# Performance work log

Hardware: AMD Instinct MI355X
Metric: run time of the kernel (lower is better)

## Reference

```python
import jax, jax.numpy as jnp
import numpy as np

DECAY = 0.8
COMMITMENT = 1.0
EPS = 1e-05


def setup_inputs() -> dict:
    key = jax.random.key(0)
    k1, k2, k3 = jax.random.split(key, 3)
    dim, n_embed = 256, 8192
    input = jax.random.normal(k1, (8, 2048, dim), dtype=jnp.float32)
    embed = jax.random.normal(k2, (dim, n_embed), dtype=jnp.float32)
    cluster_size = jnp.zeros((n_embed,), dtype=jnp.float32)
    embed_avg = jax.random.normal(k3, (dim, n_embed), dtype=jnp.float32)
    return {"input": input, "embed": embed, "cluster_size": cluster_size, "embed_avg": embed_avg}


def reference(input, embed, cluster_size, embed_avg):
    dim, n_embed = embed.shape
    flatten = input.reshape(-1, dim)  # [N, d]
    dist = (jnp.sum(flatten * flatten, axis=1, keepdims=True)
            - 2.0 * flatten @ embed
            + jnp.sum(embed * embed, axis=0, keepdims=True))  # [N, C]
    embed_ind_flat = jnp.argmin(dist, axis=1)  # [N]
    embed_ind = embed_ind_flat.reshape(input.shape[:-1])
    quantize = jnp.take(embed.T, embed_ind_flat, axis=0).reshape(input.shape)

    # training-mode EMA codebook update (onehot.sum(0) and x^T @ onehot as segment ops)
    counts = jax.ops.segment_sum(jnp.ones_like(embed_ind_flat, dtype=input.dtype),
                                 embed_ind_flat, num_segments=n_embed)  # [C]
    embed_sum = jax.ops.segment_sum(flatten, embed_ind_flat, num_segments=n_embed).T  # [d, C]
    new_cluster_size = cluster_size * DECAY + counts * (1.0 - DECAY)
    new_embed_avg = embed_avg * DECAY + embed_sum * (1.0 - DECAY)
    smoothed = (new_cluster_size + EPS) / (jnp.sum(new_cluster_size) + n_embed * EPS)
    smoothed = smoothed * jnp.sum(new_cluster_size)
    new_embed = new_embed_avg / smoothed[None, :]

    commit_loss = jnp.mean((quantize - input) ** 2) * COMMITMENT
    # straight-through (no grad here in fwd-only, values identical)
    quantize_st = input + jax.lax.stop_gradient(quantize - input)
    return quantize_st, embed_ind, commit_loss, new_embed, new_cluster_size, new_embed_avg
```

## Files before the change

kernel.cpp:

```cpp
#include <hip/hip_runtime.h>
#include <hip/hip_bf16.h>
#include <float.h>
#include <stdint.h>

#define N_ROWS 16384
#define DIM 256
#define NE 8192
#define K2 768
#define DECAY 0.8f
#define OMD 0.2f
#define EPS 1e-5f
#define NPAN 8
#define PANELC 1024

#define WS_X2     0
#define WS_EMBEDT 0
#define WS_ESUMT  2097152
#define WS_B2T    6291456
#define WS_ENORM  9437184
#define WS_COUNTS 9445376
#define WS_SMOOTH 9453568
#define WS_PV     9461760
#define WS_PI     9592832
#define WS_INDI   9723904
#define WS_LOSS   9740288
#define WS_TOTAL  9740289

#define OUT_Q    0
#define OUT_IND  4194304
#define OUT_LOSS 4210688
#define OUT_NE   4210689
#define OUT_NCS  6307841
#define OUT_NEA  6316033

typedef __attribute__((ext_vector_type(8))) short bf16x8;
typedef __attribute__((ext_vector_type(4))) float f32x4;

static __device__ __forceinline__ ushort f2bf(float f) {
    uint32_t u = __float_as_uint(f);
    uint32_t r = (u + 0x7fffu + ((u >> 16) & 1u)) >> 16;
    return (ushort)r;
}
static __device__ __forceinline__ float bf2f(ushort h) {
    return __uint_as_float(((uint32_t)h) << 16);
}
static __device__ __forceinline__ void async16(void* lds, const void* g) {
    __builtin_amdgcn_global_load_lds(
        (const __attribute__((address_space(1))) uint32_t*)g,
        (__attribute__((address_space(3))) uint32_t*)lds, 16, 0, 0);
}

__global__ __launch_bounds__(256) void convx_kernel(const float* __restrict__ x,
                                                    ushort* __restrict__ X2) {
    int i = blockIdx.x * 256 + threadIdx.x;
    int row = i >> 6, q = (i & 63) * 4;
    float4 v = *(const float4*)&x[(size_t)row * 256 + q];
    ushort4 hi, lo;
    hi.x = f2bf(v.x); hi.y = f2bf(v.y); hi.z = f2bf(v.z); hi.w = f2bf(v.w);
    lo.x = f2bf(v.x - bf2f(hi.x)); lo.y = f2bf(v.y - bf2f(hi.y));
    lo.z = f2bf(v.z - bf2f(hi.z)); lo.w = f2bf(v.w - bf2f(hi.w));
    *(ushort4*)&X2[(size_t)row * K2 + q]       = hi;
    *(ushort4*)&X2[(size_t)row * K2 + 256 + q] = lo;
    *(ushort4*)&X2[(size_t)row * K2 + 512 + q] = hi;
}

__global__ __launch_bounds__(256) void convE_kernel(const float* __restrict__ embed,
                                                    ushort* __restrict__ B2T) {
    __shared__ float t[32][33];
    int c0 = blockIdx.x * 32, d0 = blockIdx.y * 32;
    int tx = threadIdx.x & 31, ty = threadIdx.x >> 5;
    #pragma unroll
    for (int r = 0; r < 4; ++r)
        t[ty + r * 8][tx] = embed[(size_t)(d0 + ty + r * 8) * NE + c0 + tx];
    __syncthreads();
    #pragma unroll
    for (int r = 0; r < 4; ++r) {
        int c = c0 + ty + r * 8, d = d0 + tx;
        float v = t[tx][ty + r * 8];
        ushort hi = f2bf(v);
        ushort lo = f2bf(v - bf2f(hi));
        B2T[(size_t)c * K2 + d]       = hi;
        B2T[(size_t)c * K2 + 256 + d] = hi;
        B2T[(size_t)c * K2 + 512 + d] = lo;
    }
}

__global__ void enorm_kernel(const float* __restrict__ embed, float* __restrict__ enorm) {
    int c = blockIdx.x * 256 + threadIdx.x;
    float s = 0.f;
    for (int d = 0; d < DIM; ++d) { float v = embed[(size_t)d * NE + c]; s += v * v; }
    enorm[c] = s;
}

__global__ __launch_bounds__(256) void transpose_kernel(const float* __restrict__ embed,
                                                        float* __restrict__ embedT) {
    __shared__ float t[32][33];
    int c0 = blockIdx.x * 32, d0 = blockIdx.y * 32;
    int tx = threadIdx.x & 31, ty = threadIdx.x >> 5;
    #pragma unroll
    for (int r = 0; r < 4; ++r)
        t[ty + r * 8][tx] = embed[(size_t)(d0 + ty + r * 8) * NE + c0 + tx];
    __syncthreads();
    #pragma unroll
    for (int r = 0; r < 4; ++r)
        embedT[(size_t)(c0 + ty + r * 8) * DIM + d0 + tx] = t[tx][ty + r * 8];
}

__global__ __launch_bounds__(256) void argmin_mfma(
    const ushort* __restrict__ X2, const ushort* __restrict__ B2T,
    const float* __restrict__ enorm, float* __restrict__ pv, int* __restrict__ pi) {
    __shared__ ushort smem[16384];
    ushort* As = smem;
    ushort* Bs = smem + 8192;
    const int tid = threadIdx.x;
    const int lane = tid & 63;
    const int wid = tid >> 6;
    const int fl = lane & 15, fh = lane >> 4;
    const int wr0 = (wid >> 1) * 64, wc0 = (wid & 1) * 64;
    const int row0 = blockIdx.x * 128;
    const int cpan = blockIdx.y * PANELC;

    const int srow = tid >> 3;
    const int skq = (tid & 7) ^ (srow & 7);
    const ushort* aSrc[4];
    ushort* aDst[4];
    ushort* bDst[4];
    #pragma unroll
    for (int j = 0; j < 4; ++j) {
        aSrc[j] = X2 + (size_t)(row0 + srow + j * 32) * K2 + skq * 8;
        aDst[j] = As + tid * 8 + j * 2048;
        bDst[j] = Bs + tid * 8 + j * 2048;
    }

    float bestv[16]; int besti[16];
    #pragma unroll
    for (int i = 0; i < 16; ++i) { bestv[i] = FLT_MAX; besti[i] = 0; }

    int aOff[4], bOff[4];
    #pragma unroll
    for (int m = 0; m < 4; ++m) aOff[m] = (wr0 + m * 16 + fl) * 64;
    #pragma unroll
    for (int n = 0; n < 4; ++n) bOff[n] = (wc0 + n * 16 + fl) * 64;
    const int x0 = ((fh) ^ (fl & 7)) * 8;
    const int x1 = ((4 + fh) ^ (fl & 7)) * 8;

    for (int cc = 0; cc < PANELC; cc += 128) {
        const int c0 = cpan + cc;
        const ushort* bSrc[4];
        #pragma unroll
        for (int j = 0; j < 4; ++j)
            bSrc[j] = B2T + (size_t)(c0 + srow + j * 32) * K2 + skq * 8;
        f32x4 acc[4][4];
        #pragma unroll
        for (int m = 0; m < 4; ++m)
            #pragma unroll
            for (int n = 0; n < 4; ++n) acc[m][n] = (f32x4){0.f, 0.f, 0.f, 0.f};

        for (int k0 = 0; k0 < K2; k0 += 64) {
            #pragma unroll
            for (int j = 0; j < 4; ++j) async16(aDst[j], aSrc[j] + k0);
            #pragma unroll
            for (int j = 0; j < 4; ++j) async16(bDst[j], bSrc[j] + k0);
            __syncthreads();
            #pragma unroll
            for (int kk = 0; kk < 2; ++kk) {
                const int xo = kk ? x1 : x0;
                bf16x8 af[4], bfr[4];
                #pragma unroll
                for (int m = 0; m < 4; ++m) af[m] = *(const bf16x8*)&As[aOff[m] + xo];
                #pragma unroll
                for (int n = 0; n < 4; ++n) bfr[n] = *(const bf16x8*)&Bs[bOff[n] + xo];
                #pragma unroll
                for (int m = 0; m < 4; ++m)
                    #pragma unroll
                    for (int n = 0; n < 4; ++n)
                        acc[m][n] = __builtin_amdgcn_mfma_f32_16x16x32_bf16(
                            af[m], bfr[n], acc[m][n], 0, 0, 0);
            }
            __syncthreads();
        }
        #pragma unroll
        for (int n = 0; n < 4; ++n) {
            const int col = c0 + wc0 + n * 16 + fl;
            const float en = enorm[col];
            #pragma unroll
            for (int m = 0; m < 4; ++m)
                #pragma unroll
                for (int r = 0; r < 4; ++r) {
                    const float s = __builtin_fmaf(-2.f, acc[m][n][r], en);
                    const int li = m * 4 + r;
                    if (s < bestv[li]) { bestv[li] = s; besti[li] = col; }
                }
        }
    }

    __syncthreads();
    float* rv = (float*)smem;
    int* ri = (int*)(smem + 8192);
    const int eidx = (wid & 1) * 16 + fl;
    #pragma unroll
    for (int m = 0; m < 4; ++m)
        #pragma unroll
        for (int r = 0; r < 4; ++r) {
            const int rowl = wr0 + m * 16 + fh * 4 + r;
            rv[eidx * 128 + rowl] = bestv[m * 4 + r];
            ri[eidx * 128 + rowl] = besti[m * 4 + r];
        }
    __syncthreads();
    if (tid < 128) {
        float bv = rv[tid]; int bi = ri[tid];
        #pragma unroll
        for (int e = 1; e < 32; ++e) {
            float v = rv[e * 128 + tid]; int ii = ri[e * 128 + tid];
            if (v < bv || (v == bv && ii < bi)) { bv = v; bi = ii; }
        }
        pv[(size_t)(row0 + tid) * NPAN + blockIdx.y] = bv;
        pi[(size_t)(row0 + tid) * NPAN + blockIdx.y] = bi;
    }
}

__global__ __launch_bounds__(256) void rerank_kernel(
    const float* __restrict__ x, const float* __restrict__ embedT,
    const int* __restrict__ pi, float* __restrict__ out_ind, int* __restrict__ ind_i) {
    const int row = blockIdx.x * 4 + (threadIdx.x >> 6);
    const int lane = threadIdx.x & 63;
    float4 xv = *(const float4*)&x[(size_t)row * DIM + lane * 4];
    float bestd = FLT_MAX; int besti = 0;
    #pragma unroll
    for (int p = 0; p < NPAN; ++p) {
        const int c = pi[(size_t)row * NPAN + p];
        float4 e = *(const float4*)&embedT[(size_t)c * DIM + lane * 4];
        float dx = e.x - xv.x, dy = e.y - xv.y, dz = e.z - xv.z, dw = e.w - xv.w;
        float s = dx * dx + dy * dy + dz * dz + dw * dw;
        #pragma unroll
        for (int off = 32; off; off >>= 1) s += __shfl_down(s, off);
        s = __shfl(s, 0);
        if (s < bestd) { bestd = s; besti = c; }
    }
    if (lane == 0) { out_ind[row] = (float)besti; ind_i[row] = besti; }
}

__global__ __launch_bounds__(256) void gather_kernel(
    const float* __restrict__ x, const float* __restrict__ embedT,
    const int* __restrict__ ind, float* __restrict__ q_out,
    float* __restrict__ esumT, float* __restrict__ counts, float* __restrict__ loss_acc) {
    const int row = blockIdx.x * 4 + (threadIdx.x >> 6);
    const int lane = threadIdx.x & 63;
    const int idx = ind[row];
    float4 e  = *(const float4*)&embedT[(size_t)idx * DIM + lane * 4];
    float4 xv = *(const float4*)&x[(size_t)row * DIM + lane * 4];
    *(float4*)&q_out[(size_t)row * DIM + lane * 4] = e;
    float dx = e.x - xv.x, dy = e.y - xv.y, dz = e.z - xv.z, dw = e.w - xv.w;
    float s = dx * dx + dy * dy + dz * dz + dw * dw;
    #pragma unroll
    for (int off = 32; off; off >>= 1) s += __shfl_down(s, off);
    __shared__ float ls[4];
    if (lane == 0) { ls[threadIdx.x >> 6] = s; atomicAdd(&counts[idx], 1.0f); }
    atomicAdd(&esumT[(size_t)idx * DIM + lane * 4 + 0], xv.x);
    atomicAdd(&esumT[(size_t)idx * DIM + lane * 4 + 1], xv.y);
    atomicAdd(&esumT[(size_t)idx * DIM + lane * 4 + 2], xv.z);
    atomicAdd(&esumT[(size_t)idx * DIM + lane * 4 + 3], xv.w);
    __syncthreads();
    if (threadIdx.x == 0) atomicAdd(loss_acc, ls[0] + ls[1] + ls[2] + ls[3]);
}

__global__ void ncs_kernel(const float* __restrict__ cs, const float* __restrict__ counts,
                           float* __restrict__ out_ncs, float* __restrict__ total) {
    int c = blockIdx.x * 256 + threadIdx.x;
    float v = cs[c] * DECAY + counts[c] * OMD;
    out_ncs[c] = v;
    float s = v;
    #pragma unroll
    for (int off = 32; off; off >>= 1) s += __shfl_down(s, off);
    __shared__ float bs[4];
    if ((threadIdx.x & 63) == 0) bs[threadIdx.x >> 6] = s;
    __syncthreads();
    if (threadIdx.x == 0) atomicAdd(total, bs[0] + bs[1] + bs[2] + bs[3]);
}

__global__ void smooth_kernel(const float* __restrict__ out_ncs, const float* __restrict__ total,
                              float* __restrict__ smoothed, const float* __restrict__ loss_acc,
                              float* __restrict__ out_loss) {
    int c = blockIdx.x * 256 + threadIdx.x;
    float tot = *total;
    float v = out_ncs[c];
    smoothed[c] = (v + EPS) / (tot + (float)NE * EPS) * tot;
    if (blockIdx.x == 0 && threadIdx.x == 0)
        *out_loss = *loss_acc * (1.0f / ((float)N_ROWS * (float)DIM));
}

__global__ __launch_bounds__(256) void final_kernel(
    const float* __restrict__ embed_avg, const float* __restrict__ esumT,
    const float* __restrict__ smoothed, float* __restrict__ out_ne,
    float* __restrict__ out_nea) {
    __shared__ float t[32][33];
    int c0 = blockIdx.x * 32, d0 = blockIdx.y * 32;
    int tx = threadIdx.x & 31, ty = threadIdx.x >> 5;
    #pragma unroll
    for (int r = 0; r < 4; ++r)
        t[ty + r * 8][tx] = esumT[(size_t)(c0 + ty + r * 8) * DIM + d0 + tx];
    __syncthreads();
    #pragma unroll
    for (int r = 0; r < 4; ++r) {
        int d = d0 + ty + r * 8, c = c0 + tx;
        float es = t[tx][ty + r * 8];
        float ea = embed_avg[(size_t)d * NE + c] * DECAY + es * OMD;
        out_nea[(size_t)d * NE + c] = ea;
        out_ne[(size_t)d * NE + c] = ea / smoothed[c];
    }
}

extern "C" void kernel_launch(void* const* d_in, const int* in_sizes, int n_in,
                              void* d_out, int out_size, void* d_ws, size_t ws_size,
                              hipStream_t stream) {
    const float* input     = (const float*)d_in[0];
    const float* embed     = (const float*)d_in[1];
    const float* cs        = (const float*)d_in[2];
    const float* embed_avg = (const float*)d_in[3];
    float* out = (float*)d_out;
    float* ws  = (float*)d_ws;

    hipMemsetAsync(ws + WS_COUNTS, 0, (size_t)8192 * 4, stream);
    hipMemsetAsync(ws + WS_LOSS, 0, (size_t)2 * 4, stream);

    convx_kernel<<<4096, 256, 0, stream>>>(input, (ushort*)(ws + WS_X2));
    convE_kernel<<<dim3(256, 8), 256, 0, stream>>>(embed, (ushort*)(ws + WS_B2T));
    enorm_kernel<<<32, 256, 0, stream>>>(embed, ws + WS_ENORM);
    argmin_mfma<<<dim3(128, 8), 256, 0, stream>>>(
        (const ushort*)(ws + WS_X2), (const ushort*)(ws + WS_B2T), ws + WS_ENORM,
        ws + WS_PV, (int*)(ws + WS_PI));
    transpose_kernel<<<dim3(256, 8), 256, 0, stream>>>(embed, ws + WS_EMBEDT);
    hipMemsetAsync(ws + WS_ESUMT, 0, (size_t)2097152 * 4, stream);
    rerank_kernel<<<4096, 256, 0, stream>>>(input, ws + WS_EMBEDT, (int*)(ws + WS_PI),
                                            out + OUT_IND, (int*)(ws + WS_INDI));
    gather_kernel<<<4096, 256, 0, stream>>>(input, ws + WS_EMBEDT, (int*)(ws + WS_INDI),
                                            out + OUT_Q, ws + WS_ESUMT,
                                            ws + WS_COUNTS, ws + WS_LOSS);
    ncs_kernel<<<32, 256, 0, stream>>>(cs, ws + WS_COUNTS, out + OUT_NCS, ws + WS_TOTAL);
    smooth_kernel<<<32, 256, 0, stream>>>(out + OUT_NCS, ws + WS_TOTAL, ws + WS_SMOOTH,
                                          ws + WS_LOSS, out + OUT_LOSS);
    final_kernel<<<dim3(256, 8), 256, 0, stream>>>(embed_avg, ws + WS_ESUMT, ws + WS_SMOOTH,
                                                   out + OUT_NE, out + OUT_NEA);
}
```

Before: 399.0 us.

## Rewrite argmin GEMM as double-buffered 256x256 tile pipeline with interleaved prefetch

The argmin MFMA kernel now uses 512-thread blocks computing 256x256 output tiles, with LDS double buffering so the next K-slice is loaded asynchronously while MFMAs run on the current one. Each tile's reduction is split into quarter-phases with setprio hints. The per-tile argmin is done with lane shuffles into a shared reduction buffer, replacing the old per-thread best arrays, and the unused partial-value output is dropped. This aims to raise MFMA utilisation and data reuse per LDS load, at the cost of much more LDS (about 140KB) and register pressure, which limits occupancy.

```diff
diff --git a/kernel.cpp b/kernel.cpp
--- a/kernel.cpp
+++ b/kernel.cpp
@@ -11,7 +11,8 @@
 #define OMD 0.2f
 #define EPS 1e-5f
 #define NPAN 8
-#define PANELC 1024
+#define NKT 12
+#define NVT 48
 
 #define WS_X2     0
 #define WS_EMBEDT 0
@@ -20,7 +21,6 @@
 #define WS_ENORM  9437184
 #define WS_COUNTS 9445376
 #define WS_SMOOTH 9453568
-#define WS_PV     9461760
 #define WS_PI     9592832
 #define WS_INDI   9723904
 #define WS_LOSS   9740288
@@ -106,116 +106,204 @@
         embedT[(size_t)(c0 + ty + r * 8) * DIM + d0 + tx] = t[tx][ty + r * 8];
 }
 
-__global__ __launch_bounds__(256) void argmin_mfma(
+#define MFMA16(d, a, b) d = __builtin_amdgcn_mfma_f32_16x16x32_bf16(a, b, d, 0, 0, 0)
+
+__global__ __launch_bounds__(512, 2) void argmin_mfma(
     const ushort* __restrict__ X2, const ushort* __restrict__ B2T,
-    const float* __restrict__ enorm, float* __restrict__ pv, int* __restrict__ pi) {
-    __shared__ ushort smem[16384];
-    ushort* As = smem;
-    ushort* Bs = smem + 8192;
+    const float* __restrict__ enorm, int* __restrict__ pi) {
+    __shared__ ushort smem[71680];
+    ushort* const A0 = smem;
+    ushort* const A1 = smem + 16384;
+    ushort* const B0 = smem + 32768;
+    ushort* const B1 = smem + 49152;
+    float* const redv = (float*)(smem + 65536);
+    int*   const redc = (int*)(smem + 67584);
+    float* const enS  = (float*)(smem + 69632);
+
+    const int lin = blockIdx.x;
+    const int by = lin & 7, bx = lin >> 3;
+    const int row0 = bx * 256, colb = by * 1024;
+
     const int tid = threadIdx.x;
-    const int lane = tid & 63;
-    const int wid = tid >> 6;
+    const int lane = tid & 63, wid = tid >> 6;
     const int fl = lane & 15, fh = lane >> 4;
-    const int wr0 = (wid >> 1) * 64, wc0 = (wid & 1) * 64;
-    const int row0 = blockIdx.x * 128;
-    const int cpan = blockIdx.y * PANELC;
+    const int wr = wid >> 2, wc = wid & 3;
 
     const int srow = tid >> 3;
     const int skq = (tid & 7) ^ (srow & 7);
-    const ushort* aSrc[4];
-    ushort* aDst[4];
-    ushort* bDst[4];
-    #pragma unroll
-    for (int j = 0; j < 4; ++j) {
-        aSrc[j] = X2 + (size_t)(row0 + srow + j * 32) * K2 + skq * 8;
-        aDst[j] = As + tid * 8 + j * 2048;
-        bDst[j] = Bs + tid * 8 + j * 2048;
-    }
-
-    float bestv[16]; int besti[16];
-    #pragma unroll
-    for (int i = 0; i < 16; ++i) { bestv[i] = FLT_MAX; besti[i] = 0; }
-
-    int aOff[4], bOff[4];
-    #pragma unroll
-    for (int m = 0; m < 4; ++m) aOff[m] = (wr0 + m * 16 + fl) * 64;
-    #pragma unroll
-    for (int n = 0; n < 4; ++n) bOff[n] = (wc0 + n * 16 + fl) * 64;
-    const int x0 = ((fh) ^ (fl & 7)) * 8;
-    const int x1 = ((4 + fh) ^ (fl & 7)) * 8;
-
-    for (int cc = 0; cc < PANELC; cc += 128) {
-        const int c0 = cpan + cc;
-        const ushort* bSrc[4];
-        #pragma unroll
-        for (int j = 0; j < 4; ++j)
-            bSrc[j] = B2T + (size_t)(c0 + srow + j * 32) * K2 + skq * 8;
-        f32x4 acc[4][4];
+
+    enS[tid]       = enorm[colb + tid];
+    enS[tid + 512] = enorm[colb + 512 + tid];
+    redv[tid] = FLT_MAX;       redc[tid] = 0x7fffffff;
+    redv[tid + 512] = FLT_MAX; redc[tid + 512] = 0x7fffffff;
+    __builtin_amdgcn_sched_barrier(0);
+
+    const size_t aB = (size_t)(row0 + srow) * K2 + skq * 8;
+    const size_t bB = (size_t)(colb + srow) * K2 + skq * 8;
+
+    {
+        const ushort* Xa = X2 + aB;
+        const ushort* Ba = B2T + bB;
+        async16(B0 + 0 * 4096 + tid * 8, Ba + 0 * 49152);
+        async16(B0 + 1 * 4096 + tid * 8, Ba + 1 * 49152);
+        async16(B0 + 2 * 4096 + tid * 8, Ba + 2 * 49152);
+        async16(B0 + 3 * 4096 + tid * 8, Ba + 3 * 49152);
+        async16(A0 + 0 * 4096 + tid * 8, Xa + 0 * 49152);
+        async16(A0 + 2 * 4096 + tid * 8, Xa + 2 * 49152);
+        async16(A0 + 1 * 4096 + tid * 8, Xa + 1 * 49152);
+        async16(A0 + 3 * 4096 + tid * 8, Xa + 3 * 49152);
+    }
+    asm volatile("s_waitcnt vmcnt(2)" ::: "memory");
+    __builtin_amdgcn_s_barrier();
+    __builtin_amdgcn_sched_barrier(0);
+
+    const int xo0 = (fh ^ (fl & 7)) * 8;
+    const int xo1 = xo0 ^ 32;
+    const int aRB = (wr * 128 + fl) * 64;
+    const int bRB = (wc * 64 + fl) * 64;
+
+    f32x4 acc[8][4];
+    #pragma unroll
+    for (int m = 0; m < 8; ++m)
+        #pragma unroll
+        for (int n = 0; n < 4; ++n) acc[m][n] = (f32x4){0.f, 0.f, 0.f, 0.f};
+
+    bf16x8 afr[4][2], b0r[2][2], b1r[2][2];
+
+    #pragma unroll 1
+    for (int vt = 0; vt < NVT; ++vt) {
+        const int cur = vt & 1;
+        const int t = vt % NKT;
+        int nv = vt + 1; if (nv == NVT) nv = 0;
+        const int nt = nv % NKT, nct = nv / NKT;
+        const ushort* Ac = cur ? A1 : A0;
+        const ushort* Bc = cur ? B1 : B0;
+        ushort* An = cur ? A0 : A1;
+        ushort* Bn = cur ? B0 : B1;
+        const ushort* Xa = X2 + aB + (size_t)nt * 64;
+        const ushort* Ba = B2T + bB + (size_t)nct * 196608 + (size_t)nt * 64;
+
+        #pragma unroll
+        for (int m = 0; m < 4; ++m) {
+            afr[m][0] = *(const bf16x8*)&Ac[aRB + m * 1024 + xo0];
+            afr[m][1] = *(const bf16x8*)&Ac[aRB + m * 1024 + xo1];
+        }
+        #pragma unroll
+        for (int n = 0; n < 2; ++n) {
+            b0r[n][0] = *(const bf16x8*)&Bc[bRB + n * 1024 + xo0];
+            b0r[n][1] = *(const bf16x8*)&Bc[bRB + n * 1024 + xo1];
+        }
+        async16(Bn + 0 * 4096 + tid * 8, Ba + 0 * 49152);
+        async16(Bn + 1 * 4096 + tid * 8, Ba + 1 * 49152);
+        __builtin_amdgcn_s_setprio(1);
         #pragma unroll
         for (int m = 0; m < 4; ++m)
             #pragma unroll
-            for (int n = 0; n < 4; ++n) acc[m][n] = (f32x4){0.f, 0.f, 0.f, 0.f};
-
-        for (int k0 = 0; k0 < K2; k0 += 64) {
-            #pragma unroll
-            for (int j = 0; j < 4; ++j) async16(aDst[j], aSrc[j] + k0);
-            #pragma unroll
-            for (int j = 0; j < 4; ++j) async16(bDst[j], bSrc[j] + k0);
-            __syncthreads();
-            #pragma unroll
-            for (int kk = 0; kk < 2; ++kk) {
-                const int xo = kk ? x1 : x0;
-                bf16x8 af[4], bfr[4];
-                #pragma unroll
-                for (int m = 0; m < 4; ++m) af[m] = *(const bf16x8*)&As[aOff[m] + xo];
-                #pragma unroll
-                for (int n = 0; n < 4; ++n) bfr[n] = *(const bf16x8*)&Bs[bOff[n] + xo];
-                #pragma unroll
-                for (int m = 0; m < 4; ++m)
-                    #pragma unroll
-                    for (int n = 0; n < 4; ++n)
-                        acc[m][n] = __builtin_amdgcn_mfma_f32_16x16x32_bf16(
-                            af[m], bfr[n], acc[m][n], 0, 0, 0);
+            for (int n = 0; n < 2; ++n) {
+                MFMA16(acc[m][n], afr[m][0], b0r[n][0]);
+                MFMA16(acc[m][n], afr[m][1], b0r[n][1]);
             }
-            __syncthreads();
-        }
-        #pragma unroll
-        for (int n = 0; n < 4; ++n) {
-            const int col = c0 + wc0 + n * 16 + fl;
-            const float en = enorm[col];
-            #pragma unroll
-            for (int m = 0; m < 4; ++m)
+        __builtin_amdgcn_s_setprio(0);
+
+        #pragma unroll
+        for (int n = 0; n < 2; ++n) {
+            b1r[n][0] = *(const bf16x8*)&Bc[bRB + (2 + n) * 1024 + xo0];
+            b1r[n][1] = *(const bf16x8*)&Bc[bRB + (2 + n) * 1024 + xo1];
+        }
+        async16(Bn + 2 * 4096 + tid * 8, Ba + 2 * 49152);
+        async16(Bn + 3 * 4096 + tid * 8, Ba + 3 * 49152);
+        __builtin_amdgcn_s_setprio(1);
+        #pragma unroll
+        for (int m = 0; m < 4; ++m)
+            #pragma unroll
+            for (int n = 0; n < 2; ++n) {
+                MFMA16(acc[m][2 + n], afr[m][0], b1r[n][0]);
+                MFMA16(acc[m][2 + n], afr[m][1], b1r[n][1]);
+            }
+        __builtin_amdgcn_s_setprio(0);
+
+        asm volatile("s_waitcnt vmcnt(4)" ::: "memory");
+        __builtin_amdgcn_s_barrier();
+        __builtin_amdgcn_sched_barrier(0);
+        #pragma unroll
+        for (int m = 0; m < 4; ++m) {
+            afr[m][0] = *(const bf16x8*)&Ac[aRB + (4 + m) * 1024 + xo0];
+            afr[m][1] = *(const bf16x8*)&Ac[aRB + (4 + m) * 1024 + xo1];
+        }
+        async16(An + 0 * 4096 + tid * 8, Xa + 0 * 49152);
+        async16(An + 2 * 4096 + tid * 8, Xa + 2 * 49152);
+        __builtin_amdgcn_s_setprio(1);
+        #pragma unroll
+        for (int m = 0; m < 4; ++m)
+            #pragma unroll
+            for (int n = 0; n < 2; ++n) {
+                MFMA16(acc[4 + m][2 + n], afr[m][0], b1r[n][0]);
+                MFMA16(acc[4 + m][2 + n], afr[m][1], b1r[n][1]);
+            }
+        __builtin_amdgcn_s_setprio(0);
+
+        async16(An + 1 * 4096 + tid * 8, Xa + 1 * 49152);
+        async16(An + 3 * 4096 + tid * 8, Xa + 3 * 49152);
+        __builtin_amdgcn_s_setprio(1);
+        #pragma unroll
+        for (int m = 0; m < 4; ++m)
+            #pragma unroll
+            for (int n = 0; n < 2; ++n) {
+                MFMA16(acc[4 + m][n], afr[m][0], b0r[n][0]);
+                MFMA16(acc[4 + m][n], afr[m][1], b0r[n][1]);
+            }
+        __builtin_amdgcn_s_setprio(0);
+        if (t == NKT - 1) {
+            const int ct = vt / NKT;
+            const int cb = colb + ct * 256 + wc * 64;
+            float en[4];
+            #pragma unroll
+            for (int n = 0; n < 4; ++n) en[n] = enS[ct * 256 + wc * 64 + n * 16 + fl];
+            #pragma unroll
+            for (int m = 0; m < 8; ++m)
                 #pragma unroll
                 for (int r = 0; r < 4; ++r) {
-                    const float s = __builtin_fmaf(-2.f, acc[m][n][r], en);
-                    const int li = m * 4 + r;
-                    if (s < bestv[li]) { bestv[li] = s; besti[li] = col; }
+                    float bv = FLT_MAX; int bc = 0x7fffffff;
+                    #pragma unroll
+                    for (int n = 0; n < 4; ++n) {
+                        float s = __builtin_fmaf(-2.f, acc[m][n][r], en[n]);
+                        int c = cb + n * 16 + fl;
+                        if (s < bv) { bv = s; bc = c; }
+                    }
+                    #pragma unroll
+                    for (int off = 1; off < 16; off <<= 1) {
+                        float ov = __shfl_xor(bv, off, 64);
+                        int oc = __shfl_xor(bc, off, 64);
+                        if (ov < bv || (ov == bv && oc < bc)) { bv = ov; bc = oc; }
+                    }
+                    if (fl == 0) {
+                        const int slot = (wr * 128 + m * 16 + fh * 4 + r) * 4 + wc;
+                        float cv = redv[slot]; int cc = redc[slot];
+                        if (bv < cv || (bv == cv && bc < cc)) {
+                            redv[slot] = bv; redc[slot] = bc;
+                        }
+                    }
                 }
-        }
-    }
-
-    __syncthreads();
-    float* rv = (float*)smem;
-    int* ri = (int*)(smem + 8192);
-    const int eidx = (wid & 1) * 16 + fl;
-    #pragma unroll
-    for (int m = 0; m < 4; ++m)
-        #pragma unroll
-        for (int r = 0; r < 4; ++r) {
-            const int rowl = wr0 + m * 16 + fh * 4 + r;
-            rv[eidx * 128 + rowl] = bestv[m * 4 + r];
-            ri[eidx * 128 + rowl] = besti[m * 4 + r];
-        }
-    __syncthreads();
-    if (tid < 128) {
-        float bv = rv[tid]; int bi = ri[tid];
-        #pragma unroll
-        for (int e = 1; e < 32; ++e) {
-            float v = rv[e * 128 + tid]; int ii = ri[e * 128 + tid];
-            if (v < bv || (v == bv && ii < bi)) { bv = v; bi = ii; }
-        }
-        pv[(size_t)(row0 + tid) * NPAN + blockIdx.y] = bv;
-        pi[(size_t)(row0 + tid) * NPAN + blockIdx.y] = bi;
+            #pragma unroll
+            for (int m = 0; m < 8; ++m)
+                #pragma unroll
+                for (int n = 0; n < 4; ++n) acc[m][n] = (f32x4){0.f, 0.f, 0.f, 0.f};
+        }
+        asm volatile("s_waitcnt vmcnt(2)" ::: "memory");
+        __builtin_amdgcn_s_barrier();
+        __builtin_amdgcn_sched_barrier(0);
+    }
+
+    asm volatile("s_waitcnt vmcnt(0) lgkmcnt(0)" ::: "memory");
+    __builtin_amdgcn_s_barrier();
+    if (tid < 256) {
+        float bv = redv[tid * 4]; int bc = redc[tid * 4];
+        #pragma unroll
+        for (int w = 1; w < 4; ++w) {
+            float v = redv[tid * 4 + w]; int c = redc[tid * 4 + w];
+            if (v < bv || (v == bv && c < bc)) { bv = v; bc = c; }
+        }
+        pi[(size_t)(row0 + tid) * NPAN + by] = bc;
     }
 }
 
@@ -326,9 +414,9 @@
     convx_kernel<<<4096, 256, 0, stream>>>(input, (ushort*)(ws + WS_X2));
     convE_kernel<<<dim3(256, 8), 256, 0, stream>>>(embed, (ushort*)(ws + WS_B2T));
     enorm_kernel<<<32, 256, 0, stream>>>(embed, ws + WS_ENORM);
-    argmin_mfma<<<dim3(128, 8), 256, 0, stream>>>(
+    argmin_mfma<<<512, 512, 0, stream>>>(
         (const ushort*)(ws + WS_X2), (const ushort*)(ws + WS_B2T), ws + WS_ENORM,
-        ws + WS_PV, (int*)(ws + WS_PI));
+        (int*)(ws + WS_PI));
     transpose_kernel<<<dim3(256, 8), 256, 0, stream>>>(embed, ws + WS_EMBEDT);
     hipMemsetAsync(ws + WS_ESUMT, 0, (size_t)2097152 * 4, stream);
     rerank_kernel<<<4096, 256, 0, stream>>>(input, ws + WS_EMBEDT, (int*)(ws + WS_PI),
```

New measurement: 521.7 us. 1.31x slower.
